# Performance work log

Hardware: AMD Instinct MI355X
Metric: run time of the kernel (lower is better)

The kernel has to match this reference:

```python
import jax, jax.numpy as jnp
import numpy as np

F_DIM, HID, H, DQ, DV = 1024, 4096, 16, 64, 64
EPS = 1e-6

def layer_norm(x, w, b):
    mu = jnp.mean(x, axis=-1, keepdims=True)
    var = jnp.mean(jnp.square(x - mu), axis=-1, keepdims=True)
    return (x - mu) * jax.lax.rsqrt(var + EPS) * w + b

def setup_inputs() -> dict:
    key = jax.random.key(0)
    ks = jax.random.split(key, 8)
    s = 0.02
    return {
        'x': jax.random.normal(ks[0], (4, 2048, F_DIM), dtype=jnp.float32),
        'ln1_w': jnp.ones((F_DIM,), jnp.float32),
        'ln1_b': jnp.zeros((F_DIM,), jnp.float32),
        'wq_w': jax.random.normal(ks[1], (H * DQ, F_DIM), jnp.float32) * s,
        'wq_b': jnp.zeros((H * DQ,), jnp.float32),
        'wk_w': jax.random.normal(ks[2], (H * DQ, F_DIM), jnp.float32) * s,
        'wk_b': jnp.zeros((H * DQ,), jnp.float32),
        'wv_w': jax.random.normal(ks[3], (H * DV, F_DIM), jnp.float32) * s,
        'wv_b': jnp.zeros((H * DV,), jnp.float32),
        'fc_w': jax.random.normal(ks[4], (F_DIM, H * DV), jnp.float32) * s,
        'fc_b': jnp.zeros((F_DIM,), jnp.float32),
        'ln2_w': jnp.ones((F_DIM,), jnp.float32),
        'ln2_b': jnp.zeros((F_DIM,), jnp.float32),
        'fc1_w': jax.random.normal(ks[5], (HID, F_DIM), jnp.float32) * s,
        'fc1_b': jnp.zeros((HID,), jnp.float32),
        'fc2_w': jax.random.normal(ks[6], (F_DIM, HID), jnp.float32) * s,
        'fc2_b': jnp.zeros((F_DIM,), jnp.float32),
    }

def reference(x, ln1_w, ln1_b, wq_w, wq_b, wk_w, wk_b, wv_w, wv_b,
              fc_w, fc_b, ln2_w, ln2_b, fc1_w, fc1_b, fc2_w, fc2_b):
    B, S, _ = x.shape
    # --- pre-LN multi-head self-attention ---
    h = layer_norm(x, ln1_w, ln1_b)
    q = (h @ wq_w.T + wq_b).reshape(B, S, H, DQ).transpose(0, 2, 1, 3)  # [B,H,S,dq]
    k = (h @ wk_w.T + wk_b).reshape(B, S, H, DQ).transpose(0, 2, 1, 3)
    v = (h @ wv_w.T + wv_b).reshape(B, S, H, DV).transpose(0, 2, 1, 3)
    attn = jax.nn.softmax(jnp.einsum('bhqd,bhkd->bhqk', q, k) / jnp.sqrt(jnp.float32(DQ)), axis=-1)
    out = jnp.einsum('bhqk,bhkd->bhqd', attn, v).transpose(0, 2, 1, 3).reshape(B, S, H * DV)
    x = x + (out @ fc_w.T + fc_b)
    # --- pre-LN residual MLP ---
    h2 = layer_norm(x, ln2_w, ln2_b)
    ff = jax.nn.relu(h2 @ fc1_w.T + fc1_b) @ fc2_w.T + fc2_b
    return x + ff
```

## Files before the change

kernel.cpp:

```cpp
#include <hip/hip_runtime.h>

#define F_DIMC 1024
#define HIDC   4096
#define NH     16
#define SEQ    2048
#define BATCH  4
#define ROWS   (BATCH * SEQ)
#define MEG    (1u << 20)
#define QSCALE 0.18033688011112042f

typedef unsigned short u16t;
typedef __attribute__((ext_vector_type(8))) short short8;
typedef __attribute__((ext_vector_type(4))) float floatx4;
typedef __attribute__((address_space(1))) void gvoid_t;
typedef __attribute__((address_space(3))) void lvoid_t;
#define ASYNC16(g, l) __builtin_amdgcn_global_load_lds((gvoid_t*)(g), (lvoid_t*)(l), 16, 0, 0)

#if __has_builtin(__builtin_amdgcn_exp2f)
#define EXP2(x) __builtin_amdgcn_exp2f(x)
#else
#define EXP2(x) exp2f(x)
#endif

__device__ __forceinline__ u16t f2bf(float f) {
    union { float f; unsigned u; } v; v.f = f;
    unsigned r = v.u + 0x7fffu + ((v.u >> 16) & 1u);
    return (u16t)(r >> 16);
}
__device__ __forceinline__ unsigned fasu(float f) {
    union { float f; unsigned u; } v; v.f = f; return v.u;
}

__global__ __launch_bounds__(256) void ln_kernel(const float* __restrict__ x,
                                                 const float* __restrict__ w,
                                                 const float* __restrict__ b,
                                                 u16t* __restrict__ out) {
    const int row = blockIdx.x;
    const int t = threadIdx.x;
    const float* xp = x + (size_t)row * F_DIMC;

    float4 v = *(const float4*)(xp + t * 4);
    float s  = v.x + v.y + v.z + v.w;
    float ss = v.x * v.x + v.y * v.y + v.z * v.z + v.w * v.w;
    for (int off = 32; off; off >>= 1) {
        s  += __shfl_down(s, off);
        ss += __shfl_down(ss, off);
    }
    __shared__ float red[8];
    const int wid = t >> 6, lid = t & 63;
    if (lid == 0) { red[wid] = s; red[4 + wid] = ss; }
    __syncthreads();
    if (t == 0) {
        float S  = red[0] + red[1] + red[2] + red[3];
        float SS = red[4] + red[5] + red[6] + red[7];
        float mu  = S * (1.0f / F_DIMC);
        float var = SS * (1.0f / F_DIMC) - mu * mu;
        red[0] = mu;
        red[1] = rsqrtf(var + 1e-6f);
    }
    __syncthreads();
    const float mu = red[0], rs = red[1];

    float4 wv = *(const float4*)(w + t * 4);
    float4 bv = *(const float4*)(b + t * 4);
    ushort4 o = make_ushort4(f2bf((v.x - mu) * rs * wv.x + bv.x),
                             f2bf((v.y - mu) * rs * wv.y + bv.y),
                             f2bf((v.z - mu) * rs * wv.z + bv.z),
                             f2bf((v.w - mu) * rs * wv.w + bv.w));
    *(ushort4*)(out + (size_t)row * F_DIMC + t * 4) = o;
}

__global__ __launch_bounds__(256) void wconv_kernel(const float* __restrict__ w0,
        const float* __restrict__ w1, const float* __restrict__ w2,
        const float* __restrict__ w3, const float* __restrict__ w4,
        const float* __restrict__ w5, u16t* __restrict__ dst) {
    const size_t e = ((size_t)blockIdx.x * 256 + threadIdx.x) * 4;
    const float* src; size_t off;
    if      (e < 1 * MEG) { src = w0; off = e; }
    else if (e < 2 * MEG) { src = w1; off = e - 1 * MEG; }
    else if (e < 3 * MEG) { src = w2; off = e - 2 * MEG; }
    else if (e < 4 * MEG) { src = w3; off = e - 3 * MEG; }
    else if (e < 8 * MEG) { src = w4; off = e - 4 * MEG; }
    else                  { src = w5; off = e - 8 * MEG; }
    float4 f = *(const float4*)(src + off);
    *(ushort4*)(dst + e) = make_ushort4(f2bf(f.x), f2bf(f.y), f2bf(f.z), f2bf(f.w));
}

#define MFMA_Q(ACCM, ACCN, FA, FB)                                             \
    _Pragma("unroll")                                                          \
    for (int mi = 0; mi < 4; ++mi)                                             \
        _Pragma("unroll")                                                      \
        for (int ni = 0; ni < 2; ++ni) {                                       \
            acc[(ACCM) + mi][(ACCN) + ni] =                                    \
                __builtin_amdgcn_mfma_f32_16x16x32_bf16(                       \
                    FA[mi][0], FB[ni][0], acc[(ACCM) + mi][(ACCN) + ni], 0, 0, 0); \
            acc[(ACCM) + mi][(ACCN) + ni] =                                    \
                __builtin_amdgcn_mfma_f32_16x16x32_bf16(                       \
                    FA[mi][1], FB[ni][1], acc[(ACCM) + mi][(ACCN) + ni], 0, 0, 0); \
        }

#define DP8_CORE(Aq, Wq, Kdim)                                                 \
    __shared__ u16t As[2][256 * 64] __attribute__((aligned(16)));              \
    __shared__ u16t Bs[2][256 * 64] __attribute__((aligned(16)));              \
    const int t = threadIdx.x;                                                 \
    const int lane = t & 63;                                                   \
    const int wave = t >> 6;                                                   \
    const int wr = wave >> 2, wc = wave & 3;                                   \
    const int fm = lane & 15, fq = lane >> 4;                                  \
    const int nwg = gridDim.x;                                                 \
    const int swzb = (blockIdx.x & 7) * (nwg >> 3) + (blockIdx.x >> 3);        \
    const int m0 = (swzb & 31) * 256;                \
    const int n0 = (swzb >> 5) * 256;                                          \
       \
    const int beta0 = t, beta1 = t + 512;                                      \
    const int r0 = beta0 >> 3, j0 = (beta0 & 7) ^ (r0 & 7);                    \
    const int r1 = beta1 >> 3, j1 = (beta1 & 7) ^ (r1 & 7);                    \
    const u16t* aP0 = (Aq) + (size_t)(m0 + r0) * (Kdim) + j0 * 8;              \
    const u16t* aP1 = (Aq) + (size_t)(m0 + r1) * (Kdim) + j1 * 8;              \
    const u16t* bP0 = (Wq) + (size_t)(n0 + r0) * (Kdim) + j0 * 8;              \
    const u16t* bP1 = (Wq) + (size_t)(n0 + r1) * (Kdim) + j1 * 8;              \
    const size_t aH = (size_t)128 * (Kdim);      \
    const int l0 = beta0 * 8, l1 = beta1 * 8;                                  \
        \
    int aoff[2], boff[2];                                                      \
    _Pragma("unroll")                                                          \
    for (int ks = 0; ks < 2; ++ks) {                                           \
        const int sw = ((ks * 4 + fq) ^ (fm & 7)) * 8;                         \
        aoff[ks] = wr * 8192 + fm * 64 + sw;                                   \
        boff[ks] = (wc >> 1) * 8192 + ((wc & 1) * 64 + fm) * 64 + sw;          \
    }                                                                          \
    const int NT = (Kdim) / 64;                                                \
                         \
    { u16t* d = &As[0][0];    ASYNC16(aP0, d + l0); ASYNC16(aP1, d + l1); }    \
    { u16t* d = &As[0][8192]; ASYNC16(aP0 + aH, d + l0); ASYNC16(aP1 + aH, d + l1); } \
    { u16t* d = &Bs[0][0];    ASYNC16(bP0, d + l0); ASYNC16(bP1, d + l1); }    \
    { u16t* d = &Bs[0][8192]; ASYNC16(bP0 + aH, d + l0); ASYNC16(bP1 + aH, d + l1); } \
    { u16t* d = &Bs[1][0];    ASYNC16(bP0 + 64, d + l0); ASYNC16(bP1 + 64, d + l1); } \
    { u16t* d = &Bs[1][8192]; ASYNC16(bP0 + aH + 64, d + l0); ASYNC16(bP1 + aH + 64, d + l1); } \
    asm volatile("s_waitcnt vmcnt(4)" ::: "memory");         \
    __builtin_amdgcn_s_barrier();                                              \
    __builtin_amdgcn_sched_barrier(0);                                         \
    floatx4 acc[8][4] = {};                                                    \
    short8 fa[4][2], fbL[2][2], fbH[2][2];                                     \
    for (int T = 0; T < NT; ++T) {                                             \
        const u16t* Ab = &As[T & 1][0];                                        \
        const u16t* Bb = &Bs[T & 1][0];                                        \
        const size_t kA = (size_t)(T + 1) * 64;                                \
        const size_t kB = (size_t)(T + 2) * 64;                                \
                                    \
        _Pragma("unroll")                                                      \
        for (int mi = 0; mi < 4; ++mi) {                                       \
            fa[mi][0] = *(const short8*)(Ab + aoff[0] + mi * 1024);            \
            fa[mi][1] = *(const short8*)(Ab + aoff[1] + mi * 1024);            \
        }                                                                      \
        _Pragma("unroll")                                                      \
        for (int ni = 0; ni < 2; ++ni) {                                       \
            fbL[ni][0] = *(const short8*)(Bb + boff[0] + ni * 1024);           \
            fbL[ni][1] = *(const short8*)(Bb + boff[1] + ni * 1024);           \
        }                                                                      \
        __builtin_amdgcn_sched_barrier(0);                                     \
        if (T + 1 < NT) {                                                      \
            u16t* d = &As[(T + 1) & 1][0];                                     \
            ASYNC16(aP0 + kA, d + l0); ASYNC16(aP1 + kA, d + l1);              \
        }                                                                      \
        asm volatile("s_waitcnt lgkmcnt(8)" ::: "memory");                     \
        __builtin_amdgcn_sched_barrier(0);                                     \
        __builtin_amdgcn_s_barrier();                                          \
        asm volatile("s_waitcnt lgkmcnt(0)" ::: "memory");                     \
        __builtin_amdgcn_sched_barrier(0);                                     \
        __builtin_amdgcn_s_setprio(1);                                         \
        MFMA_Q(0, 0, fa, fbL)                                                  \
        __builtin_amdgcn_s_setprio(0);                                         \
        __builtin_amdgcn_sched_barrier(0);                                     \
        __builtin_amdgcn_s_barrier();                                          \
                                    \
        _Pragma("unroll")                                                      \
        for (int ni = 0; ni < 2; ++ni) {                                       \
            fbH[ni][0] = *(const short8*)(Bb + boff[0] + 2048 + ni * 1024);    \
            fbH[ni][1] = *(const short8*)(Bb + boff[1] + 2048 + ni * 1024);    \
        }                                                                      \
        __builtin_amdgcn_sched_barrier(0);                                     \
        if (T + 1 < NT) {                                                      \
            u16t* d = &As[(T + 1) & 1][8192];                                  \
            ASYNC16(aP0 + aH + kA, d + l0); ASYNC16(aP1 + aH + kA, d + l1);    \
        }                                                                      \
        __builtin_amdgcn_sched_barrier(0);                                     \
        __builtin_amdgcn_s_barrier();                                          \
        asm volatile("s_waitcnt lgkmcnt(0)" ::: "memory");                     \
        __builtin_amdgcn_sched_barrier(0);                                     \
        __builtin_amdgcn_s_setprio(1);                                         \
        MFMA_Q(0, 2, fa, fbH)                                                  \
        __builtin_amdgcn_s_setprio(0);                                         \
        __builtin_amdgcn_sched_barrier(0);                                     \
        __builtin_amdgcn_s_barrier();                                          \
                                    \
        _Pragma("unroll")                                                      \
        for (int mi = 0; mi < 4; ++mi) {                                       \
            fa[mi][0] = *(const short8*)(Ab + aoff[0] + 4096 + mi * 1024);     \
            fa[mi][1] = *(const short8*)(Ab + aoff[1] + 4096 + mi * 1024);     \
        }                                                                      \
        __builtin_amdgcn_sched_barrier(0);                                     \
        if (T + 2 < NT) {                                                      \
            u16t* d = &Bs[T & 1][0];                                           \
            ASYNC16(bP0 + kB, d + l0); ASYNC16(bP1 + kB, d + l1);              \
        }                                                                      \
        __builtin_amdgcn_sched_barrier(0);                                     \
        __builtin_amdgcn_s_barrier();                                          \
        asm volatile("s_waitcnt lgkmcnt(0)" ::: "memory");                     \
        __builtin_amdgcn_sched_barrier(0);                                     \
        __builtin_amdgcn_s_setprio(1);                                         \
        MFMA_Q(4, 0, fa, fbL)                                                  \
        __builtin_amdgcn_s_setprio(0);                                         \
        __builtin_amdgcn_sched_barrier(0);                                     \
        __builtin_amdgcn_s_barrier();                                          \
                                    \
        if (T + 2 < NT) {                                                      \
            u16t* d = &Bs[T & 1][8192];                                        \
            ASYNC16(bP0 + aH + kB, d + l0); ASYNC16(bP1 + aH + kB, d + l1);    \
            asm volatile("s_waitcnt vmcnt(4)" ::: "memory");                   \
        } else {                                                               \
            asm volatile("s_waitcnt vmcnt(0)" ::: "memory");                   \
        }                                                                      \
        __builtin_amdgcn_sched_barrier(0);                                     \
        __builtin_amdgcn_s_barrier();                                          \
        __builtin_amdgcn_sched_barrier(0);                                     \
        __builtin_amdgcn_s_setprio(1);                                         \
        MFMA_Q(4, 2, fa, fbH)                                                  \
        __builtin_amdgcn_s_setprio(0);                                         \
        __builtin_amdgcn_sched_barrier(0);                                     \
        __builtin_amdgcn_s_barrier();                                          \
    }

template <bool RELU, bool RES, bool BF16OUT>
__global__ __launch_bounds__(512, 2) void gemm_dp(const u16t* __restrict__ A,
                                                  const u16t* __restrict__ W,
                                                  const float* __restrict__ bias,
                                                  const float* res, void* Cout,
                                                  int N, int K) {
    DP8_CORE(A, W, K)
    float bl[4];
#pragma unroll
    for (int ni = 0; ni < 4; ++ni) bl[ni] = bias[n0 + wc * 64 + ni * 16 + fm];
#pragma unroll
    for (int mi = 0; mi < 8; ++mi) {
#pragma unroll
        for (int ni = 0; ni < 4; ++ni) {
            const int col = n0 + wc * 64 + ni * 16 + fm;
#pragma unroll
            for (int r = 0; r < 4; ++r) {
                const int row = m0 + wr * 128 + mi * 16 + fq * 4 + r;
                const size_t off = (size_t)row * N + col;
                float c = acc[mi][ni][r] + bl[ni];
                if (RELU) c = fmaxf(c, 0.0f);
                if (RES)  c += res[off];
                if (BF16OUT) ((u16t*)Cout)[off] = f2bf(c);
                else         ((float*)Cout)[off] = c;
            }
        }
    }
}

__global__ __launch_bounds__(512, 2) void gemm_qkv(const u16t* __restrict__ A,
        const u16t* __restrict__ W,
        const float* __restrict__ wq_b, const float* __restrict__ wk_b,
        const float* __restrict__ wv_b,
        u16t* __restrict__ qb, u16t* __restrict__ kb, u16t* __restrict__ vtb) {
    DP8_CORE(A, W, F_DIMC)
    const int which = n0 >> 10;
    const int nb = n0 & 1023;
    const float* bias = which == 0 ? wq_b : which == 1 ? wk_b : wv_b;
    float bl[4];
#pragma unroll
    for (int ni = 0; ni < 4; ++ni) bl[ni] = bias[nb + wc * 64 + ni * 16 + fm];

    if (which == 2) {
#pragma unroll
        for (int mi = 0; mi < 8; ++mi)
#pragma unroll
            for (int ni = 0; ni < 4; ++ni) {
                const int col = nb + wc * 64 + ni * 16 + fm;
                const int row0 = m0 + wr * 128 + mi * 16 + fq * 4;
                ushort4 pk = make_ushort4(f2bf(acc[mi][ni][0] + bl[ni]),
                                          f2bf(acc[mi][ni][1] + bl[ni]),
                                          f2bf(acc[mi][ni][2] + bl[ni]),
                                          f2bf(acc[mi][ni][3] + bl[ni]));
                *(ushort4*)(vtb + (size_t)col * ROWS + row0) = pk;
            }
    } else {
        u16t* dst = (which == 0) ? qb : kb;
        const float sc2 = (which == 0) ? QSCALE : 1.0f;
#pragma unroll
        for (int mi = 0; mi < 8; ++mi)
#pragma unroll
            for (int ni = 0; ni < 4; ++ni) {
                const int col = nb + wc * 64 + ni * 16 + fm;
#pragma unroll
                for (int r = 0; r < 4; ++r) {
                    const int row = m0 + wr * 128 + mi * 16 + fq * 4 + r;
                    dst[(size_t)row * F_DIMC + col] = f2bf((acc[mi][ni][r] + bl[ni]) * sc2);
                }
            }
    }
}

__global__ __launch_bounds__(256, 4) void attn_mfma(const u16t* __restrict__ qb,
        const u16t* __restrict__ kbuf, const u16t* __restrict__ vtb,
        u16t* __restrict__ ab) {
    __shared__ u16t Kt[2][64 * 64] __attribute__((aligned(16)));
    __shared__ u16t Vs[64 * 64] __attribute__((aligned(16)));
    __shared__ u16t QP[128 * 64] __attribute__((aligned(16)));

    const int t = threadIdx.x;
    const int lane = t & 63;
    const int wave = t >> 6;
    const int l15 = lane & 15, q4 = lane >> 4;
    const int q0 = blockIdx.x * 128;
    const int bh = blockIdx.y;
    const int b = bh >> 4, hh = bh & 15;

#pragma unroll
    for (int c = 0; c < 4; ++c) {
        const int beta = c * 256 + t;
        const int r = beta >> 3, o = (beta & 7) ^ (r & 7);
        ASYNC16(qb + (size_t)(b * SEQ + q0 + r) * F_DIMC + hh * 64 + o * 8,
                QP + beta * 8);
    }
    const u16t* kg = kbuf + (size_t)(b * SEQ) * F_DIMC + hh * 64;
    const u16t* vg = vtb + (size_t)(hh * 64) * ROWS + b * SEQ;

    const int sb0 = t, sb1 = t + 256;
    const int sr0 = sb0 >> 3, so0 = (sb0 & 7) ^ (sr0 & 7);
    const int sr1 = sb1 >> 3, so1 = (sb1 & 7) ^ (sr1 & 7);
    const u16t* kp0 = kg + (size_t)sr0 * F_DIMC + so0 * 8;
    const u16t* kp1 = kg + (size_t)sr1 * F_DIMC + so1 * 8;
    const u16t* vp0 = vg + (size_t)sr0 * ROWS + so0 * 8;
    const u16t* vp1 = vg + (size_t)sr1 * ROWS + so1 * 8;

    ASYNC16(kp0, Kt[0] + sb0 * 8);
    ASYNC16(kp1, Kt[0] + sb1 * 8);
    ASYNC16(vp0, Vs + sb0 * 8);
    ASYNC16(vp1, Vs + sb1 * 8);
    kp0 += 64 * F_DIMC; kp1 += 64 * F_DIMC; vp0 += 64; vp1 += 64;
    __syncthreads();

    short8 fqr[2][2];
#pragma unroll
    for (int mt = 0; mt < 2; ++mt)
#pragma unroll
        for (int ks = 0; ks < 2; ++ks) {
            const int m = wave * 32 + mt * 16 + l15;
            const int oct = ks * 4 + q4;
            fqr[mt][ks] = *(const short8*)(QP + (m * 8 + (oct ^ (m & 7))) * 8);
        }

    short8 ones;
#pragma unroll
    for (int i = 0; i < 8; ++i) ones[i] = (short)0x3F80;

    floatx4 oacc[2][4] = {};
    floatx4 lacc[2] = {};

    for (int it = 0; it < SEQ / 64; ++it) {
        if (it + 1 < SEQ / 64) {
            u16t* kd = Kt[(it + 1) & 1];
            ASYNC16(kp0, kd + sb0 * 8);
            ASYNC16(kp1, kd + sb1 * 8);
            kp0 += 64 * F_DIMC; kp1 += 64 * F_DIMC;
        }
        const u16t* kcur = Kt[it & 1];

        short8 fk[4][2];
#pragma unroll
        for (int nt = 0; nt < 4; ++nt)
#pragma unroll
            for (int ks = 0; ks < 2; ++ks) {
                const int kr = nt * 16 + l15;
                const int oct = ks * 4 + q4;
                fk[nt][ks] = *(const short8*)(kcur + (kr * 8 + (oct ^ (kr & 7))) * 8);
            }
        floatx4 st[2][4] = {};
#pragma unroll
        for (int mt = 0; mt < 2; ++mt)
#pragma unroll
            for (int nt = 0; nt < 4; ++nt) {
                st[mt][nt] = __builtin_amdgcn_mfma_f32_16x16x32_bf16(
                    fk[nt][0], fqr[mt][0], st[mt][nt], 0, 0, 0);
                st[mt][nt] = __builtin_amdgcn_mfma_f32_16x16x32_bf16(
                    fk[nt][1], fqr[mt][1], st[mt][nt], 0, 0, 0);
            }

#pragma unroll
        for (int mt = 0; mt < 2; ++mt)
#pragma unroll
            for (int nt = 0; nt < 4; ++nt) {
                const float p0 = EXP2(st[mt][nt][0]);
                const float p1 = EXP2(st[mt][nt][1]);
                const float p2 = EXP2(st[mt][nt][2]);
                const float p3 = EXP2(st[mt][nt][3]);
                const unsigned lo = __builtin_amdgcn_perm(fasu(p1), fasu(p0), 0x07060302u);
                const unsigned hi = __builtin_amdgcn_perm(fasu(p3), fasu(p2), 0x07060302u);
                const int m = wave * 32 + mt * 16 + l15;
                const int logb = nt * 2 + (q4 >> 1);
                *(uint2*)(QP + (m * 8 + (logb ^ (m & 7))) * 8 + (q4 & 1) * 4) =
                    make_uint2(lo, hi);
            }

        __syncthreads();

        short8 fp[2][2], fv[4][2];
#pragma unroll
        for (int mt = 0; mt < 2; ++mt)
#pragma unroll
            for (int ks = 0; ks < 2; ++ks) {
                const int m = wave * 32 + mt * 16 + l15;
                const int oct = ks * 4 + q4;
                fp[mt][ks] = *(const short8*)(QP + (m * 8 + (oct ^ (m & 7))) * 8);
            }
#pragma unroll
        for (int nd = 0; nd < 4; ++nd)
#pragma unroll
            for (int ks = 0; ks < 2; ++ks) {
                const int d = nd * 16 + l15;
                const int oct = ks * 4 + q4;
                fv[nd][ks] = *(const short8*)(Vs + (d * 8 + (oct ^ (d & 7))) * 8);
            }
#pragma unroll
        for (int mt = 0; mt < 2; ++mt) {
#pragma unroll
            for (int nd = 0; nd < 4; ++nd) {
                oacc[mt][nd] = __builtin_amdgcn_mfma_f32_16x16x32_bf16(
                    fp[mt][0], fv[nd][0], oacc[mt][nd], 0, 0, 0);
                oacc[mt][nd] = __builtin_amdgcn_mfma_f32_16x16x32_bf16(
                    fp[mt][1], fv[nd][1], oacc[mt][nd], 0, 0, 0);
            }
            lacc[mt] = __builtin_amdgcn_mfma_f32_16x16x32_bf16(
                fp[mt][0], ones, lacc[mt], 0, 0, 0);
            lacc[mt] = __builtin_amdgcn_mfma_f32_16x16x32_bf16(
                fp[mt][1], ones, lacc[mt], 0, 0, 0);
        }

        __syncthreads();
        if (it + 1 < SEQ / 64) {
            ASYNC16(vp0, Vs + sb0 * 8);
            ASYNC16(vp1, Vs + sb1 * 8);
            vp0 += 64; vp1 += 64;
        }
    }

#pragma unroll
    for (int mt = 0; mt < 2; ++mt) {
        floatx4 rinv;
#pragma unroll
        for (int r = 0; r < 4; ++r) rinv[r] = 1.0f / lacc[mt][r];
#pragma unroll
        for (int nd = 0; nd < 4; ++nd)
#pragma unroll
            for (int r = 0; r < 4; ++r) {
                const int row = b * SEQ + q0 + wave * 32 + mt * 16 + q4 * 4 + r;
                const int col = hh * 64 + nd * 16 + l15;
                ab[(size_t)row * F_DIMC + col] = f2bf(oacc[mt][nd][r] * rinv[r]);
            }
    }
}

extern "C" void kernel_launch(void* const* d_in, const int* in_sizes, int n_in,
                              void* d_out, int out_size, void* d_ws, size_t ws_size,
                              hipStream_t stream) {
    const float* x     = (const float*)d_in[0];
    const float* ln1_w = (const float*)d_in[1];
    const float* ln1_b = (const float*)d_in[2];
    const float* wq_w  = (const float*)d_in[3];
    const float* wq_b  = (const float*)d_in[4];
    const float* wk_w  = (const float*)d_in[5];
    const float* wk_b  = (const float*)d_in[6];
    const float* wv_w  = (const float*)d_in[7];
    const float* wv_b  = (const float*)d_in[8];
    const float* fc_w  = (const float*)d_in[9];
    const float* fc_b  = (const float*)d_in[10];
    const float* ln2_w = (const float*)d_in[11];
    const float* ln2_b = (const float*)d_in[12];
    const float* fc1_w = (const float*)d_in[13];
    const float* fc1_b = (const float*)d_in[14];
    const float* fc2_w = (const float*)d_in[15];
    const float* fc2_b = (const float*)d_in[16];

    float* out = (float*)d_out;
    u16t*  ws  = (u16t*)d_ws;

    u16t* wbuf = ws;
    u16t* bwqkv = wbuf;
    u16t* bwfc = wbuf + 3 * MEG;
    u16t* bwf1 = wbuf + 4 * MEG;
    u16t* bwf2 = wbuf + 8 * MEG;
    u16t* h    = wbuf + 12 * MEG;
    u16t* qb   = h + 8 * MEG;
    u16t* kb   = qb + 8 * MEG;
    u16t* vtb  = kb + 8 * MEG;
    u16t* ab   = vtb + 8 * MEG;
    u16t* ff   = qb;

    const dim3 blk(256);
    const dim3 blk512(512);
    const int gQKV = 32 * (3072 / 256);
    const int gF   = 32 * (F_DIMC / 256);
    const int gH   = 32 * (HIDC / 256);

    wconv_kernel<<<12 * MEG / 1024, blk, 0, stream>>>(wq_w, wk_w, wv_w, fc_w, fc1_w, fc2_w, wbuf);
    ln_kernel<<<ROWS, blk, 0, stream>>>(x, ln1_w, ln1_b, h);
    gemm_qkv<<<gQKV, blk512, 0, stream>>>(h, bwqkv, wq_b, wk_b, wv_b, qb, kb, vtb);
    attn_mfma<<<dim3(SEQ / 128, BATCH * NH), blk, 0, stream>>>(qb, kb, vtb, ab);
    gemm_dp<false, true, false><<<gF, blk512, 0, stream>>>(ab, bwfc, fc_b, x, out, F_DIMC, F_DIMC);
    ln_kernel<<<ROWS, blk, 0, stream>>>(out, ln2_w, ln2_b, h);
    gemm_dp<true, false, true><<<gH, blk512, 0, stream>>>(h, bwf1, fc1_b, nullptr, ff, HIDC, F_DIMC);
    gemm_dp<false, true, false><<<gF, blk512, 0, stream>>>(ff, bwf2, fc2_b, out, out, F_DIMC, HIDC);
}
```

Measured before the change: 567.5 us.

## Unroll GEMM K-loop by two with a reordered async LDS prefetch schedule

The bf16 MFMA GEMM main loop is unrolled over pairs of K-tiles with fixed double-buffer base pointers. The global-to-LDS async loads are re-sequenced per half-tile, with the next pair prefetched only while enough K-tiles remain. The explicit lgkmcnt waits and most sched_barriers are dropped, leaving the compiler to place LDS waits and reorder instructions. The goal is less per-iteration index and wait overhead and better overlap of loads with MFMAs. The cost is weaker control over scheduling and a subtler buffer-hazard ordering.

Result: slower. 583.8 us (+2.9%).

```diff
diff --git a/kernel.cpp b/kernel.cpp
--- a/kernel.cpp
+++ b/kernel.cpp
@@ -99,9 +99,23 @@
                     FA[mi][1], FB[ni][1], acc[(ACCM) + mi][(ACCN) + ni], 0, 0, 0); \
         }
 
+#define STAGE_A(par, h, kt) do {                                               \
+        u16t* d_ = &As[par][(h) * 8192];                                       \
+        ASYNC16(aP0 + (h) * aH + (size_t)(kt) * 64, d_ + l0);                  \
+        ASYNC16(aP1 + (h) * aH + (size_t)(kt) * 64, d_ + l1); } while (0)
+#define STAGE_B(par, h, kt) do {                                               \
+        u16t* d_ = &Bs[par][(h) * 8192];                                       \
+        ASYNC16(bP0 + (h) * aH + (size_t)(kt) * 64, d_ + l0);                  \
+        ASYNC16(bP1 + (h) * aH + (size_t)(kt) * 64, d_ + l1); } while (0)
+#define VMCNT4 asm volatile("s_waitcnt vmcnt(4)" ::: "memory")
+#define VMCNT0 asm volatile("s_waitcnt vmcnt(0)" ::: "memory")
+#define BAR()  __builtin_amdgcn_s_barrier()
+#define PRIO1() __builtin_amdgcn_s_setprio(1)
+#define PRIO0() __builtin_amdgcn_s_setprio(0)
+
 #define DP8_CORE(Aq, Wq, Kdim)                                                 \
-    __shared__ u16t As[2][256 * 64] __attribute__((aligned(16)));              \
-    __shared__ u16t Bs[2][256 * 64] __attribute__((aligned(16)));              \
+    __shared__ u16t As[2][2 * 8192] __attribute__((aligned(16)));              \
+    __shared__ u16t Bs[2][2 * 8192] __attribute__((aligned(16)));              \
     const int t = threadIdx.x;                                                 \
     const int lane = t & 63;                                                   \
     const int wave = t >> 6;                                                   \
@@ -111,7 +125,7 @@
     const int swzb = (blockIdx.x & 7) * (nwg >> 3) + (blockIdx.x >> 3);        \
     const int m0 = (swzb & 31) * 256;                \
     const int n0 = (swzb >> 5) * 256;                                          \
-       \
+          \
     const int beta0 = t, beta1 = t + 512;                                      \
     const int r0 = beta0 >> 3, j0 = (beta0 & 7) ^ (r0 & 7);                    \
     const int r1 = beta1 >> 3, j1 = (beta1 & 7) ^ (r1 & 7);                    \
@@ -119,9 +133,9 @@
     const u16t* aP1 = (Aq) + (size_t)(m0 + r1) * (Kdim) + j1 * 8;              \
     const u16t* bP0 = (Wq) + (size_t)(n0 + r0) * (Kdim) + j0 * 8;              \
     const u16t* bP1 = (Wq) + (size_t)(n0 + r1) * (Kdim) + j1 * 8;              \
-    const size_t aH = (size_t)128 * (Kdim);      \
+    const size_t aH = (size_t)128 * (Kdim);       \
     const int l0 = beta0 * 8, l1 = beta1 * 8;                                  \
-        \
+                   \
     int aoff[2], boff[2];                                                      \
     _Pragma("unroll")                                                          \
     for (int ks = 0; ks < 2; ++ks) {                                           \
@@ -130,105 +144,100 @@
         boff[ks] = (wc >> 1) * 8192 + ((wc & 1) * 64 + fm) * 64 + sw;          \
     }                                                                          \
     const int NT = (Kdim) / 64;                                                \
-                         \
-    { u16t* d = &As[0][0];    ASYNC16(aP0, d + l0); ASYNC16(aP1, d + l1); }    \
-    { u16t* d = &As[0][8192]; ASYNC16(aP0 + aH, d + l0); ASYNC16(aP1 + aH, d + l1); } \
-    { u16t* d = &Bs[0][0];    ASYNC16(bP0, d + l0); ASYNC16(bP1, d + l1); }    \
-    { u16t* d = &Bs[0][8192]; ASYNC16(bP0 + aH, d + l0); ASYNC16(bP1 + aH, d + l1); } \
-    { u16t* d = &Bs[1][0];    ASYNC16(bP0 + 64, d + l0); ASYNC16(bP1 + 64, d + l1); } \
-    { u16t* d = &Bs[1][8192]; ASYNC16(bP0 + aH + 64, d + l0); ASYNC16(bP1 + aH + 64, d + l1); } \
-    asm volatile("s_waitcnt vmcnt(4)" ::: "memory");         \
-    __builtin_amdgcn_s_barrier();                                              \
-    __builtin_amdgcn_sched_barrier(0);                                         \
+                       \
+    STAGE_A(0, 0, 0); STAGE_A(0, 1, 0); STAGE_B(0, 0, 0); STAGE_B(0, 1, 0);    \
+    STAGE_B(1, 0, 1); STAGE_A(1, 0, 1);                                        \
+    VMCNT4;                                                                    \
+    BAR();                                                                     \
     floatx4 acc[8][4] = {};                                                    \
     short8 fa[4][2], fbL[2][2], fbH[2][2];                                     \
-    for (int T = 0; T < NT; ++T) {                                             \
-        const u16t* Ab = &As[T & 1][0];                                        \
-        const u16t* Bb = &Bs[T & 1][0];                                        \
-        const size_t kA = (size_t)(T + 1) * 64;                                \
-        const size_t kB = (size_t)(T + 2) * 64;                                \
-                                    \
+    for (int u = 0; u < NT / 2; ++u) {                                         \
+        const int U = 2 * u;                                                   \
+        const bool full = (U + 4 <= NT);                                       \
+        const u16t* A0 = &As[0][0];  const u16t* B0 = &Bs[0][0];               \
+        const u16t* A1 = &As[1][0];  const u16t* B1 = &Bs[1][0];               \
+             \
         _Pragma("unroll")                                                      \
         for (int mi = 0; mi < 4; ++mi) {                                       \
-            fa[mi][0] = *(const short8*)(Ab + aoff[0] + mi * 1024);            \
-            fa[mi][1] = *(const short8*)(Ab + aoff[1] + mi * 1024);            \
+            fa[mi][0] = *(const short8*)(A0 + aoff[0] + mi * 1024);            \
+            fa[mi][1] = *(const short8*)(A0 + aoff[1] + mi * 1024);            \
         }                                                                      \
         _Pragma("unroll")                                                      \
         for (int ni = 0; ni < 2; ++ni) {                                       \
-            fbL[ni][0] = *(const short8*)(Bb + boff[0] + ni * 1024);           \
-            fbL[ni][1] = *(const short8*)(Bb + boff[1] + ni * 1024);           \
-        }                                                                      \
-        __builtin_amdgcn_sched_barrier(0);                                     \
-        if (T + 1 < NT) {                                                      \
-            u16t* d = &As[(T + 1) & 1][0];                                     \
-            ASYNC16(aP0 + kA, d + l0); ASYNC16(aP1 + kA, d + l1);              \
-        }                                                                      \
-        asm volatile("s_waitcnt lgkmcnt(8)" ::: "memory");                     \
-        __builtin_amdgcn_sched_barrier(0);                                     \
-        __builtin_amdgcn_s_barrier();                                          \
-        asm volatile("s_waitcnt lgkmcnt(0)" ::: "memory");                     \
-        __builtin_amdgcn_sched_barrier(0);                                     \
-        __builtin_amdgcn_s_setprio(1);                                         \
-        MFMA_Q(0, 0, fa, fbL)                                                  \
-        __builtin_amdgcn_s_setprio(0);                                         \
-        __builtin_amdgcn_sched_barrier(0);                                     \
-        __builtin_amdgcn_s_barrier();                                          \
-                                    \
+            fbL[ni][0] = *(const short8*)(B0 + boff[0] + ni * 1024);           \
+            fbL[ni][1] = *(const short8*)(B0 + boff[1] + ni * 1024);           \
+        }                                                                      \
+        STAGE_A(1, 1, U + 1);                                                  \
+        BAR();                                                                 \
+        PRIO1(); MFMA_Q(0, 0, fa, fbL) PRIO0();                                \
+        BAR();                                                                 \
+                      \
         _Pragma("unroll")                                                      \
         for (int ni = 0; ni < 2; ++ni) {                                       \
-            fbH[ni][0] = *(const short8*)(Bb + boff[0] + 2048 + ni * 1024);    \
-            fbH[ni][1] = *(const short8*)(Bb + boff[1] + 2048 + ni * 1024);    \
-        }                                                                      \
-        __builtin_amdgcn_sched_barrier(0);                                     \
-        if (T + 1 < NT) {                                                      \
-            u16t* d = &As[(T + 1) & 1][8192];                                  \
-            ASYNC16(aP0 + aH + kA, d + l0); ASYNC16(aP1 + aH + kA, d + l1);    \
-        }                                                                      \
-        __builtin_amdgcn_sched_barrier(0);                                     \
-        __builtin_amdgcn_s_barrier();                                          \
-        asm volatile("s_waitcnt lgkmcnt(0)" ::: "memory");                     \
-        __builtin_amdgcn_sched_barrier(0);                                     \
-        __builtin_amdgcn_s_setprio(1);                                         \
-        MFMA_Q(0, 2, fa, fbH)                                                  \
-        __builtin_amdgcn_s_setprio(0);                                         \
-        __builtin_amdgcn_sched_barrier(0);                                     \
-        __builtin_amdgcn_s_barrier();                                          \
-                                    \
+            fbH[ni][0] = *(const short8*)(B0 + boff[0] + 2048 + ni * 1024);    \
+            fbH[ni][1] = *(const short8*)(B0 + boff[1] + 2048 + ni * 1024);    \
+        }                                                                      \
+        STAGE_B(1, 1, U + 1);                                                  \
+        BAR();                                                                 \
+        PRIO1(); MFMA_Q(0, 2, fa, fbH) PRIO0();                                \
+        BAR();                                                                 \
+                      \
         _Pragma("unroll")                                                      \
         for (int mi = 0; mi < 4; ++mi) {                                       \
-            fa[mi][0] = *(const short8*)(Ab + aoff[0] + 4096 + mi * 1024);     \
-            fa[mi][1] = *(const short8*)(Ab + aoff[1] + 4096 + mi * 1024);     \
-        }                                                                      \
-        __builtin_amdgcn_sched_barrier(0);                                     \
-        if (T + 2 < NT) {                                                      \
-            u16t* d = &Bs[T & 1][0];                                           \
-            ASYNC16(bP0 + kB, d + l0); ASYNC16(bP1 + kB, d + l1);              \
-        }                                                                      \
-        __builtin_amdgcn_sched_barrier(0);                                     \
-        __builtin_amdgcn_s_barrier();                                          \
-        asm volatile("s_waitcnt lgkmcnt(0)" ::: "memory");                     \
-        __builtin_amdgcn_sched_barrier(0);                                     \
-        __builtin_amdgcn_s_setprio(1);                                         \
-        MFMA_Q(4, 0, fa, fbL)                                                  \
-        __builtin_amdgcn_s_setprio(0);                                         \
-        __builtin_amdgcn_sched_barrier(0);                                     \
-        __builtin_amdgcn_s_barrier();                                          \
-                                    \
-        if (T + 2 < NT) {                                                      \
-            u16t* d = &Bs[T & 1][8192];                                        \
-            ASYNC16(bP0 + aH + kB, d + l0); ASYNC16(bP1 + aH + kB, d + l1);    \
-            asm volatile("s_waitcnt vmcnt(4)" ::: "memory");                   \
-        } else {                                                               \
-            asm volatile("s_waitcnt vmcnt(0)" ::: "memory");                   \
-        }                                                                      \
-        __builtin_amdgcn_sched_barrier(0);                                     \
-        __builtin_amdgcn_s_barrier();                                          \
-        __builtin_amdgcn_sched_barrier(0);                                     \
-        __builtin_amdgcn_s_setprio(1);                                         \
-        MFMA_Q(4, 2, fa, fbH)                                                  \
-        __builtin_amdgcn_s_setprio(0);                                         \
-        __builtin_amdgcn_sched_barrier(0);                                     \
-        __builtin_amdgcn_s_barrier();                                          \
+            fa[mi][0] = *(const short8*)(A0 + aoff[0] + 4096 + mi * 1024);     \
+            fa[mi][1] = *(const short8*)(A0 + aoff[1] + 4096 + mi * 1024);     \
+        }                                                                      \
+        if (full) STAGE_B(0, 0, U + 2);                                        \
+        BAR();                                                                 \
+        PRIO1(); MFMA_Q(4, 0, fa, fbL) PRIO0();                                \
+        BAR();                                                                 \
+              \
+        if (full) STAGE_A(0, 0, U + 2);                                        \
+        BAR();                                                                 \
+        PRIO1(); MFMA_Q(4, 2, fa, fbH) PRIO0();                                \
+        if (full) { VMCNT4; } else { VMCNT0; }                                 \
+        BAR();                                                                 \
+               \
+        _Pragma("unroll")                                                      \
+        for (int mi = 0; mi < 4; ++mi) {                                       \
+            fa[mi][0] = *(const short8*)(A1 + aoff[0] + mi * 1024);            \
+            fa[mi][1] = *(const short8*)(A1 + aoff[1] + mi * 1024);            \
+        }                                                                      \
+        _Pragma("unroll")                                                      \
+        for (int ni = 0; ni < 2; ++ni) {                                       \
+            fbL[ni][0] = *(const short8*)(B1 + boff[0] + ni * 1024);           \
+            fbL[ni][1] = *(const short8*)(B1 + boff[1] + ni * 1024);           \
+        }                                                                      \
+        if (full) STAGE_A(0, 1, U + 2);                                        \
+        BAR();                                                                 \
+        PRIO1(); MFMA_Q(0, 0, fa, fbL) PRIO0();                                \
+        BAR();                                                                 \
+                          \
+        _Pragma("unroll")                                                      \
+        for (int ni = 0; ni < 2; ++ni) {                                       \
+            fbH[ni][0] = *(const short8*)(B1 + boff[0] + 2048 + ni * 1024);    \
+            fbH[ni][1] = *(const short8*)(B1 + boff[1] + 2048 + ni * 1024);    \
+        }                                                                      \
+        if (full) STAGE_B(0, 1, U + 2);                                        \
+        BAR();                                                                 \
+        PRIO1(); MFMA_Q(0, 2, fa, fbH) PRIO0();                                \
+        BAR();                                                                 \
+                          \
+        _Pragma("unroll")                                                      \
+        for (int mi = 0; mi < 4; ++mi) {                                       \
+            fa[mi][0] = *(const short8*)(A1 + aoff[0] + 4096 + mi * 1024);     \
+            fa[mi][1] = *(const short8*)(A1 + aoff[1] + 4096 + mi * 1024);     \
+        }                                                                      \
+        if (full) STAGE_B(1, 0, U + 3);                                        \
+        BAR();                                                                 \
+        PRIO1(); MFMA_Q(4, 0, fa, fbL) PRIO0();                                \
+        BAR();                                                                 \
+              \
+        if (full) STAGE_A(1, 0, U + 3);                                        \
+        BAR();                                                                 \
+        PRIO1(); MFMA_Q(4, 2, fa, fbH) PRIO0();                                \
+        if (full) { VMCNT4; } else { VMCNT0; }                                 \
+        BAR();                                                                 \
     }
 
 template <bool RELU, bool RES, bool BF16OUT>
```
